# Kernel tuning notes

Hardware: AMD Instinct MI355X
Metric: run time of the kernel (lower is better)

The kernel has to match this reference:

```python
import jax, jax.numpy as jnp
import numpy as np

TEMPERATURE = 0.1
NUM_CLASSES = 21
L2_EPS = 1e-12   # torch F.normalize eps
NEG = -1e9       # masking value for invalid (absent-class) logit slots


def setup_inputs() -> dict:
    key = jax.random.key(0)
    k1, k2 = jax.random.split(key)
    features = jax.random.normal(k1, (16, 512, 64, 64), dtype=jnp.float32)
    labels = jax.random.randint(k2, (16, 513, 513), 0, NUM_CLASSES, dtype=jnp.int32)
    return {"features": features, "labels": labels}


def reference(features, labels):
    B, D, H, W = features.shape
    C = NUM_CLASSES
    # torch: F.interpolate(labels.float()[:,None], (H,W), mode='bilinear').squeeze(1).long()
    lab = jax.image.resize(labels.astype(jnp.float32)[:, None], (B, 1, H, W),
                           method="bilinear", antialias=False)
    lab = lab[:, 0].astype(jnp.int32)                     # [B,H,W]

    # per-image, per-class masked feature pooling (segment reduce)
    masks = (lab[:, None, :, :] == jnp.arange(C)[None, :, None, None]).astype(features.dtype)  # [B,C,H,W]
    sums = jnp.einsum('bdhw,bchw->bcd', features, masks)  # [B,C,D]
    norms = jnp.linalg.norm(sums, axis=-1, keepdims=True)
    protos = sums / jnp.maximum(norms, L2_EPS)            # normalized prototypes [B,C,D]
    pres = masks.sum((2, 3)) > 0                          # [B,C] class present in image

    # all pairwise prototype dots: S[c,e,i,j] = <proto[i,c], proto[j,e]> / T
    S = jnp.einsum('icd,jed->ceij', protos, protos) / TEMPERATURE  # [C,C,B,B]
    presT = pres.T                                        # [C,B]
    valid = presT[:, None, :, None] & presT[None, :, None, :]       # [C,C,B,B]
    masked = jnp.where(valid, S, NEG)

    idx = jnp.arange(C)
    diag = masked[idx, idx]                               # [C,B,B] positive block S[c,c]
    dvalid = valid[idx, idx]                              # [C,B,B]

    # logits for class c = concat(p_block, all n_blocks) -> diag block appears twice
    lse_diag = jax.nn.logsumexp(diag, axis=(1, 2))        # [C]
    lse_all = jax.nn.logsumexp(masked, axis=(1, 2, 3))    # [C]
    lse = jnp.logaddexp(lse_diag, lse_all)                # [C]

    cnt = dvalid.sum((1, 2))
    pos_mean = jnp.where(dvalid, diag, 0.0).sum((1, 2)) / jnp.maximum(cnt, 1)

    cls_present = pres.any(0)                             # [C]
    loss = jnp.sum(jnp.where(cls_present, lse - pos_mean, 0.0))
    return loss
```

## Files before the change

### kernel.cpp

```cpp
#include <hip/hip_runtime.h>
#include <cstdint>
#include <cstddef>

#define NUM_C 21
#define NROW 336
#define N2   (NROW * NROW)
#define KSLABS 16

typedef __attribute__((ext_vector_type(8))) short short8;
typedef __attribute__((ext_vector_type(4))) float f32x4;
typedef __attribute__((ext_vector_type(16))) float f32x16;
typedef __attribute__((ext_vector_type(4))) int int4v;

union frag_u { int4v i; short8 s; };
__device__ __forceinline__ short8 mk_frag(uint32_t a0, uint32_t a1, uint32_t a2, uint32_t a3) {
    frag_u u; u.i = int4v{(int)a0, (int)a1, (int)a2, (int)a3}; return u.s;
}
__device__ __forceinline__ uint32_t mask_pair(uint32_t eL, uint32_t eH, uint32_t c) {
    return (eL == c ? 0x3F80u : 0u) | (eH == c ? 0x3F800000u : 0u);
}
__device__ __forceinline__ void load_lds16(const float* src, float* dst) {
    __builtin_amdgcn_global_load_lds((const __attribute__((address_space(1))) void*)src,
                                     (__attribute__((address_space(3))) void*)dst, 16, 0, 2);
}

__global__ __launch_bounds__(256) void k1_resize_hist(const int* __restrict__ labels,
                                                      uint8_t* __restrict__ lab,
                                                      int* __restrict__ countsPart,
                                                      float* __restrict__ out) {
    int b = blockIdx.x >> 4, strip = blockIdx.x & 15;
    if (blockIdx.x == 0 && threadIdx.x == 0) out[0] = 0.0f;
    __shared__ int hist[NUM_C];
    if (threadIdx.x < NUM_C) hist[threadIdx.x] = 0;
    __syncthreads();

    int p = strip * 256 + threadIdx.x;
    int y = p >> 6, x = p & 63;
    const int* L = labels + (size_t)b * 263169;
    float sy = (y + 0.5f) * 8.015625f - 0.5f;
    float sx = (x + 0.5f) * 8.015625f - 0.5f;
    int y0 = (int)sy; float fy = sy - (float)y0;
    int x0 = (int)sx; float fx = sx - (float)x0;
    const int* r0 = L + y0 * 513 + x0;
    float L00 = (float)__builtin_nontemporal_load(r0);
    float L01 = (float)__builtin_nontemporal_load(r0 + 1);
    float L10 = (float)__builtin_nontemporal_load(r0 + 513);
    float L11 = (float)__builtin_nontemporal_load(r0 + 514);
    float v0 = (1.0f - fx) * L00 + fx * L01;
    float v1 = (1.0f - fx) * L10 + fx * L11;
    float val = (1.0f - fy) * v0 + fy * v1;
    int c = (int)val;
    lab[b * 4096 + p] = (uint8_t)c;
    atomicAdd(&hist[c], 1);
    __syncthreads();
    if (threadIdx.x < NUM_C) countsPart[blockIdx.x * NUM_C + threadIdx.x] = hist[threadIdx.x];
}

__global__ __launch_bounds__(256) void k2_sums(const float* __restrict__ feat,
                                               const uint8_t* __restrict__ lab,
                                               float* __restrict__ sums_part) {
    int bid = blockIdx.x;
    int b = bid >> 6, dg = (bid >> 2) & 15, ks = bid & 3;
    int t = threadIdx.x, wv = t >> 6, lane = t & 63;
    int g = lane >> 5;
    uint32_t c = lane & 31;
    __shared__ float tile[32 * 260];

    const float* fbase = feat + ((size_t)(b * 512 + dg * 32)) * 4096 + ks * 1024;
    const uint8_t* lbase = lab + b * 4096 + ks * 1024;

    f32x16 acc;
#pragma unroll
    for (int j = 0; j < 16; ++j) acc[j] = 0.0f;

    for (int slab = 0; slab < 4; ++slab) {
        int px0 = slab * 256;
#pragma unroll
        for (int rr = 0; rr < 8; ++rr) {
            int r = wv * 8 + rr;
            load_lds16(fbase + (size_t)r * 4096 + px0 + lane * 4, &tile[r * 260]);
        }
        __syncthreads();

        const uint8_t* lp = lbase + px0 + wv * 64 + g * 8;
        const float* lrow = &tile[(lane & 31) * 260 + wv * 64 + g * 8];
#pragma unroll
        for (int ch = 0; ch < 4; ++ch) {
            f32x4 fA = *(const f32x4*)(lrow + ch * 16);
            f32x4 fB = *(const f32x4*)(lrow + ch * 16 + 4);
            uint2 wl = *(const uint2*)(lp + ch * 16);

            uint32_t u0 = __float_as_uint(fA[0]), u1 = __float_as_uint(fA[1]),
                     u2 = __float_as_uint(fA[2]), u3 = __float_as_uint(fA[3]),
                     u4 = __float_as_uint(fB[0]), u5 = __float_as_uint(fB[1]),
                     u6 = __float_as_uint(fB[2]), u7 = __float_as_uint(fB[3]);
            short8 bHi = mk_frag(__builtin_amdgcn_perm(u1, u0, 0x07060302u),
                                 __builtin_amdgcn_perm(u3, u2, 0x07060302u),
                                 __builtin_amdgcn_perm(u5, u4, 0x07060302u),
                                 __builtin_amdgcn_perm(u7, u6, 0x07060302u));
            float t0 = fA[0] - __uint_as_float(u0 & 0xFFFF0000u);
            float t1 = fA[1] - __uint_as_float(u1 & 0xFFFF0000u);
            float t2 = fA[2] - __uint_as_float(u2 & 0xFFFF0000u);
            float t3 = fA[3] - __uint_as_float(u3 & 0xFFFF0000u);
            float t4 = fB[0] - __uint_as_float(u4 & 0xFFFF0000u);
            float t5 = fB[1] - __uint_as_float(u5 & 0xFFFF0000u);
            float t6 = fB[2] - __uint_as_float(u6 & 0xFFFF0000u);
            float t7 = fB[3] - __uint_as_float(u7 & 0xFFFF0000u);
            short8 bLo = mk_frag(
                __builtin_amdgcn_perm(__float_as_uint(t1), __float_as_uint(t0), 0x07060302u),
                __builtin_amdgcn_perm(__float_as_uint(t3), __float_as_uint(t2), 0x07060302u),
                __builtin_amdgcn_perm(__float_as_uint(t5), __float_as_uint(t4), 0x07060302u),
                __builtin_amdgcn_perm(__float_as_uint(t7), __float_as_uint(t6), 0x07060302u));

            uint32_t e0 = wl.x & 255u, e1 = (wl.x >> 8) & 255u,
                     e2 = (wl.x >> 16) & 255u, e3 = wl.x >> 24;
            uint32_t e4 = wl.y & 255u, e5 = (wl.y >> 8) & 255u,
                     e6 = (wl.y >> 16) & 255u, e7 = wl.y >> 24;
            short8 a = mk_frag(mask_pair(e0, e1, c), mask_pair(e2, e3, c),
                               mask_pair(e4, e5, c), mask_pair(e6, e7, c));

            acc = __builtin_amdgcn_mfma_f32_32x32x16_bf16(a, bHi, acc, 0, 0, 0);
            acc = __builtin_amdgcn_mfma_f32_32x32x16_bf16(a, bLo, acc, 0, 0, 0);
        }
        __syncthreads();
    }

    float* sp = sums_part + (size_t)(ks * 4 + wv) * NROW * 512;
    int d = dg * 32 + (lane & 31);
    int rb = 4 * g;
#pragma unroll
    for (int j = 0; j < 16; ++j) {
        int row = (j & 3) + 8 * (j >> 2) + rb;
        if (row < NUM_C) sp[(size_t)(row * 16 + b) * 512 + d] = acc[j];
    }
}

__global__ __launch_bounds__(256) void k3_fold(const float4* __restrict__ part,
                                               float4* __restrict__ sums) {
    int idx = blockIdx.x * 256 + threadIdx.x;
    float4 s = part[idx];
#pragma unroll
    for (int q = 1; q < KSLABS; ++q) {
        float4 v = part[q * 43008 + idx];
        s.x += v.x; s.y += v.y; s.z += v.z; s.w += v.w;
    }
    sums[idx] = s;
}

__global__ __launch_bounds__(64) void k4_gram(const float* __restrict__ sums,
                                              float* __restrict__ gpart) {
    int row0 = blockIdx.x * 32, col0 = blockIdx.y * 32, k0 = blockIdx.z * 64;
    __shared__ float A[32 * 66], Bt[32 * 66];
    int t = threadIdx.x;
    int row = t >> 1, kk0 = (t & 1) * 32;
#pragma unroll
    for (int q = 0; q < 8; ++q) {
        int kk = kk0 + q * 4;
        int ra = row0 + row, rb = col0 + row;
        float4 va = (ra < NROW) ? *(const float4*)&sums[(size_t)ra * 512 + k0 + kk]
                                : make_float4(0.f, 0.f, 0.f, 0.f);
        float4 vb = (rb < NROW) ? *(const float4*)&sums[(size_t)rb * 512 + k0 + kk]
                                : make_float4(0.f, 0.f, 0.f, 0.f);
        *(float2*)&A[row * 66 + kk]      = make_float2(va.x, va.y);
        *(float2*)&A[row * 66 + kk + 2]  = make_float2(va.z, va.w);
        *(float2*)&Bt[row * 66 + kk]     = make_float2(vb.x, vb.y);
        *(float2*)&Bt[row * 66 + kk + 2] = make_float2(vb.z, vb.w);
    }
    __syncthreads();
    int ty = t >> 3, tx = t & 7;
    float acc[4][4] = {};
    for (int kk = 0; kk < 64; kk += 2) {
        float2 a[4], bb[4];
#pragma unroll
        for (int u = 0; u < 4; ++u) {
            a[u]  = *(const float2*)&A[(ty * 4 + u) * 66 + kk];
            bb[u] = *(const float2*)&Bt[(tx * 4 + u) * 66 + kk];
        }
#pragma unroll
        for (int u = 0; u < 4; ++u)
#pragma unroll
            for (int v = 0; v < 4; ++v)
                acc[u][v] += a[u].x * bb[v].x + a[u].y * bb[v].y;
    }
    float* gp = gpart + (size_t)blockIdx.z * N2;
#pragma unroll
    for (int u = 0; u < 4; ++u) {
        int r1 = row0 + ty * 4 + u;
        if (r1 >= NROW) continue;
        int r2 = col0 + tx * 4;
        if (r2 + 3 < NROW) {
            *(float4*)&gp[(size_t)r1 * NROW + r2] =
                make_float4(acc[u][0], acc[u][1], acc[u][2], acc[u][3]);
        } else {
#pragma unroll
            for (int v = 0; v < 4; ++v)
                if (r2 + v < NROW) gp[(size_t)r1 * NROW + r2 + v] = acc[u][v];
        }
    }
}

__global__ __launch_bounds__(1024) void k5_loss(const float* __restrict__ gpart,
                                                const int* __restrict__ countsPart,
                                                float* __restrict__ out) {
    int c = blockIdx.x, t = threadIdx.x;
    int wv = t >> 6, lane = t & 63;
    __shared__ float invnL[NROW];
    __shared__ uint8_t presL[NROW];
    __shared__ float redE[16], redD[16], redL[16];

    for (int r = t; r < NROW; r += 1024) {
        float ss = 0.0f;
#pragma unroll
        for (int s = 0; s < 8; ++s) ss += gpart[(size_t)s * N2 + (size_t)r * 337];
        invnL[r] = 1.0f / fmaxf(sqrtf(ss), 1e-12f);
        int img = r & 15, cls = r >> 4;
        int cnt = 0;
#pragma unroll
        for (int s = 0; s < 16; ++s) cnt += countsPart[(img * 16 + s) * NUM_C + cls];
        presL[r] = cnt > 0 ? 1 : 0;
    }
    __syncthreads();

    int nc = 0;
#pragma unroll
    for (int j = 0; j < 16; ++j) nc += presL[c * 16 + j];
    if (nc == 0) return;

    float eS = 0.0f, dE = 0.0f, dL = 0.0f;
    for (int idx = t; idx < 16 * NROW; idx += 1024) {
        int i = idx / NROW, r2 = idx - i * NROW;
        int r1 = c * 16 + i;
        float g = 0.0f;
#pragma unroll
        for (int s = 0; s < 8; ++s) g += gpart[(size_t)s * N2 + (size_t)r1 * NROW + r2];
        if (presL[r1] && presL[r2]) {
            float sv = g * invnL[r1] * invnL[r2] * 10.0f;
            float e = expf(sv - 10.0f);
            eS += e;
            if ((r2 >> 4) == c) { dE += e; dL += sv; }
        }
    }
#pragma unroll
    for (int off = 32; off >= 1; off >>= 1) {
        eS += __shfl_xor(eS, off, 64);
        dE += __shfl_xor(dE, off, 64);
        dL += __shfl_xor(dL, off, 64);
    }
    if (lane == 0) { redE[wv] = eS; redD[wv] = dE; redL[wv] = dL; }
    __syncthreads();
    if (t == 0) {
        float E = 0, D = 0, Ln = 0;
#pragma unroll
        for (int w = 0; w < 16; ++w) { E += redE[w]; D += redD[w]; Ln += redL[w]; }
        float lse = 10.0f + logf(E + D);
        float posMean = Ln / (float)(nc * nc);
        atomicAdd(out, lse - posMean);
    }
}

extern "C" void kernel_launch(void* const* d_in, const int* in_sizes, int n_in,
                              void* d_out, int out_size, void* d_ws, size_t ws_size,
                              hipStream_t stream) {
    const float* features = (const float*)d_in[0];
    const int* labels = (const int*)d_in[1];
    char* ws = (char*)d_ws;

    uint8_t* lab     = (uint8_t*)ws;
    int* countsPart  = (int*)(ws + 65536);
    float* sums_part = (float*)(ws + 87040);
    float* sums      = (float*)(ws + 87040 + 11010048);
    float* gpart     = (float*)(ws + 87040 + 11010048 + 688128);
    float* out       = (float*)d_out;

    k1_resize_hist<<<256, 256, 0, stream>>>(labels, lab, countsPart, out);
    k2_sums<<<1024, 256, 0, stream>>>(features, lab, sums_part);
    k3_fold<<<168, 256, 0, stream>>>((const float4*)sums_part, (float4*)sums);
    k4_gram<<<dim3(11, 11, 8), 64, 0, stream>>>(sums, gpart);
    k5_loss<<<21, 1024, 0, stream>>>(gpart, countsPart, out);
}
```

Before: 217.7 us.

## Double-buffer feature tiles in LDS with XOR swizzle and halve K-split

The masked-sum kernel now double-buffers its LDS feature tiles, issuing the asynchronous global-to-LDS loads for the next slab while MFMAs consume the current one. Padding is replaced by an XOR swizzle to avoid bank conflicts. Each block covers twice as many pixels, which halves the grid, the number of partial-sum slabs and the fold kernel's work. The trade is fewer blocks for latency hiding and twice the LDS per block. The prefetch is also issued before the buffer's previous readers have finished, so its ordering depends on the existing barrier.

```diff
diff --git a/kernel.cpp b/kernel.cpp
--- a/kernel.cpp
+++ b/kernel.cpp
@@ -5,7 +5,7 @@
 #define NUM_C 21
 #define NROW 336
 #define N2   (NROW * NROW)
-#define KSLABS 16
+#define KSLABS 8
 
 typedef __attribute__((ext_vector_type(8))) short short8;
 typedef __attribute__((ext_vector_type(4))) float f32x4;
@@ -60,34 +60,45 @@
                                                const uint8_t* __restrict__ lab,
                                                float* __restrict__ sums_part) {
     int bid = blockIdx.x;
-    int b = bid >> 6, dg = (bid >> 2) & 15, ks = bid & 3;
+    int b = bid >> 5, dg = (bid >> 1) & 15, ks = bid & 1;
     int t = threadIdx.x, wv = t >> 6, lane = t & 63;
     int g = lane >> 5;
+    int r = lane & 31;
     uint32_t c = lane & 31;
-    __shared__ float tile[32 * 260];
-
-    const float* fbase = feat + ((size_t)(b * 512 + dg * 32)) * 4096 + ks * 1024;
-    const uint8_t* lbase = lab + b * 4096 + ks * 1024;
+    __shared__ float tile[2][32][256];
+
+    const float* fbase = feat + ((size_t)(b * 512 + dg * 32)) * 4096 + ks * 2048;
+    const uint8_t* lbase = lab + b * 4096 + ks * 2048;
 
     f32x16 acc;
 #pragma unroll
     for (int j = 0; j < 16; ++j) acc[j] = 0.0f;
 
-    for (int slab = 0; slab < 4; ++slab) {
-        int px0 = slab * 256;
-#pragma unroll
-        for (int rr = 0; rr < 8; ++rr) {
-            int r = wv * 8 + rr;
-            load_lds16(fbase + (size_t)r * 4096 + px0 + lane * 4, &tile[r * 260]);
-        }
-        __syncthreads();
-
-        const uint8_t* lp = lbase + px0 + wv * 64 + g * 8;
-        const float* lrow = &tile[(lane & 31) * 260 + wv * 64 + g * 8];
+#define STAGE(bb, slab)                                                              \
+    {                                                                                \
+        int px0 = (slab) * 256;                                                      \
+        _Pragma("unroll")                                                            \
+        for (int rr = 0; rr < 8; ++rr) {                                             \
+            int row = wv * 8 + rr;                                                   \
+            load_lds16(fbase + (size_t)row * 4096 + px0 + ((lane ^ row) << 2),       \
+                       &tile[bb][row][0]);                                           \
+        }                                                                            \
+    }
+
+    STAGE(0, 0)
+    __syncthreads();
+    int buf = 0;
+
+    for (int slab = 0; slab < 8; ++slab) {
+        if (slab < 7) STAGE(buf ^ 1, slab + 1)
+
+        const uint8_t* lp = lbase + slab * 256 + wv * 64 + g * 8;
+        const float* trow = &tile[buf][r][0];
 #pragma unroll
         for (int ch = 0; ch < 4; ++ch) {
-            f32x4 fA = *(const f32x4*)(lrow + ch * 16);
-            f32x4 fB = *(const f32x4*)(lrow + ch * 16 + 4);
+            int sA = wv * 16 + ch * 4 + g * 2;
+            f32x4 fA = *(const f32x4*)(trow + ((sA ^ r) << 2));
+            f32x4 fB = *(const f32x4*)(trow + (((sA + 1) ^ r) << 2));
             uint2 wl = *(const uint2*)(lp + ch * 16);
 
             uint32_t u0 = __float_as_uint(fA[0]), u1 = __float_as_uint(fA[1]),
@@ -123,7 +134,9 @@
             acc = __builtin_amdgcn_mfma_f32_32x32x16_bf16(a, bLo, acc, 0, 0, 0);
         }
         __syncthreads();
-    }
+        buf ^= 1;
+    }
+#undef STAGE
 
     float* sp = sums_part + (size_t)(ks * 4 + wv) * NROW * 512;
     int d = dg * 32 + (lane & 31);
@@ -268,12 +281,12 @@
     uint8_t* lab     = (uint8_t*)ws;
     int* countsPart  = (int*)(ws + 65536);
     float* sums_part = (float*)(ws + 87040);
-    float* sums      = (float*)(ws + 87040 + 11010048);
-    float* gpart     = (float*)(ws + 87040 + 11010048 + 688128);
+    float* sums      = (float*)(ws + 87040 + 5505024);
+    float* gpart     = (float*)(ws + 87040 + 5505024 + 688128);
     float* out       = (float*)d_out;
 
     k1_resize_hist<<<256, 256, 0, stream>>>(labels, lab, countsPart, out);
-    k2_sums<<<1024, 256, 0, stream>>>(features, lab, sums_part);
+    k2_sums<<<512, 256, 0, stream>>>(features, lab, sums_part);
     k3_fold<<<168, 256, 0, stream>>>((const float4*)sums_part, (float4*)sums);
     k4_gram<<<dim3(11, 11, 8), 64, 0, stream>>>(sums, gpart);
     k5_loss<<<21, 1024, 0, stream>>>(gpart, countsPart, out);
```

New measurement: 226.6 us. +4.1%, slower.
